# Kernel tuning notes

Hardware: AMD Instinct MI355X
Metric: run time of the kernel (lower is better)

The kernel has to match this reference:

```python
import jax, jax.numpy as jnp
import numpy as np

H = 128          # hidden_dim
NC = 100000      # num_cst
NV = 100000      # num_val
E = 1600000      # num edges
EPS = 1e-5


def _layernorm(x, g, b):
    mu = x.mean(-1, keepdims=True)
    var = x.var(-1, keepdims=True)
    return (x - mu) / jnp.sqrt(var + EPS) * g + b


def setup_inputs() -> dict:
    key = jax.random.key(0)
    ks = jax.random.split(key, 16)
    s = 0.05
    return {
        "x_val": jax.random.normal(ks[0], (NV, H), jnp.float32),
        "r_cst": jax.random.normal(ks[1], (NC, H), jnp.float32),
        "cst_edges": jax.random.randint(ks[2], (2, E), 0, NC, dtype=jnp.int32),
        "LE": jax.random.randint(ks[3], (E,), 0, 2, dtype=jnp.int32),
        "PE": jax.random.randint(ks[4], (E,), 0, 2, dtype=jnp.int32),
        "num_cst": NC,
        "num_val": NV,
        # cst_send: Linear(H,H,bias) -> ReLU -> Linear(H,4H,no bias) -> LayerNorm(4H)
        "W1": jax.random.normal(ks[5], (H, H), jnp.float32) * s,
        "b1": jax.random.normal(ks[6], (H,), jnp.float32) * s,
        "W2": jax.random.normal(ks[7], (H, 4 * H), jnp.float32) * s,
        "g1": jnp.ones((4 * H,), jnp.float32),
        "bt1": jnp.zeros((4 * H,), jnp.float32),
        # val_rec: Linear(H,H,bias) -> ReLU -> Linear(H,H,no bias) -> LayerNorm(H)
        "W3": jax.random.normal(ks[8], (H, H), jnp.float32) * s,
        "b3": jax.random.normal(ks[9], (H,), jnp.float32) * s,
        "W4": jax.random.normal(ks[10], (H, H), jnp.float32) * s,
        "g2": jnp.ones((H,), jnp.float32),
        "bt2": jnp.zeros((H,), jnp.float32),
    }


def reference(x_val, r_cst, cst_edges, LE, PE, num_cst, num_val,
              W1, b1, W2, g1, bt1, W3, b3, W4, g2, bt2):
    # cst_send MLP: [NC, H] -> [NC, 4H], LayerNorm over 4H, then view as [4*NC, H]
    m = _layernorm(jnp.maximum(r_cst @ W1 + b1, 0.0) @ W2, g1, bt1)
    m = m.reshape(4 * num_cst, H)
    # each edge picks one of the 4 message slots of its constraint
    out_idx = 4 * cst_edges[0] + 2 * LE + PE   # [E]
    in_idx = cst_edges[1]                      # [E]
    msg = m[out_idx]                           # [E, H] gather
    r_val = jax.ops.segment_sum(msg, in_idx, num_segments=num_val)  # [NV, H]
    # val_rec MLP on (x_val + r_val) with residual
    h = x_val + r_val
    return _layernorm(jnp.maximum(h @ W3 + b3, 0.0) @ W4, g2, bt2) + x_val
```

## Files before the change

### kernel.cpp

```cpp
#include <hip/hip_runtime.h>
#include <hip/hip_bf16.h>

#define H 128
#define H4 512
#define BM 16

typedef __bf16 bf16x8 __attribute__((ext_vector_type(8)));
typedef float f32x4 __attribute__((ext_vector_type(4)));

__device__ inline f32x4 mfma16(bf16x8 a, bf16x8 b, f32x4 c) {
  return __builtin_amdgcn_mfma_f32_16x16x32_bf16(a, b, c, 0, 0, 0);
}

__global__ __launch_bounds__(256) void pack_kernel(const float* __restrict__ W, int K, int N,
                                                   __bf16* __restrict__ hi,
                                                   __bf16* __restrict__ lo) {
  int idx = blockIdx.x * 256 + threadIdx.x;
  int total = (N >> 4) * (K >> 5) * 64;
  if (idx >= total) return;
  int lane = idx & 63;
  int tile = idx >> 6;
  int KT = K >> 5;
  int nt = tile / KT, kt = tile - nt * KT;
  int col = nt * 16 + (lane & 15);
  int k0 = kt * 32 + (lane >> 4) * 8;
#pragma unroll
  for (int i = 0; i < 8; ++i) {
    float x = W[(long)(k0 + i) * N + col];
    __bf16 h = (__bf16)x;
    hi[(long)idx * 8 + i] = h;
    lo[(long)idx * 8 + i] = (__bf16)(x - (float)h);
  }
}

__global__ __launch_bounds__(256) void copy_kernel(const float4* __restrict__ src,
                                                   float4* __restrict__ dst, int n4) {
  int i = blockIdx.x * 256 + threadIdx.x;
  int stride = gridDim.x * 256;
  for (; i < n4; i += stride) dst[i] = src[i];
}

__global__ __launch_bounds__(256) void cst_mlp_mfma(
    const float* __restrict__ r_cst,
    const __bf16* __restrict__ W1h, const __bf16* __restrict__ W1l,
    const float* __restrict__ b1,
    const __bf16* __restrict__ W2h, const __bf16* __restrict__ W2l,
    const float* __restrict__ g1, const float* __restrict__ bt1,
    float* __restrict__ m) {
  __shared__ float As[BM][132];
  __shared__ float Cs[BM][132];
  __shared__ float Ds[BM][H4];
  __shared__ float mu_s[BM], rs_s[BM];

  const int tid = threadIdx.x;
  const int wave = tid >> 6, lane = tid & 63;
  const long row0 = (long)blockIdx.x * BM;

  {
    const float4* src = (const float4*)(r_cst + row0 * H);
#pragma unroll
    for (int i = 0; i < 2; ++i) {
      int idx = tid + i * 256;
      int r = idx >> 5, c4 = idx & 31;
      *(float4*)&As[r][c4 * 4] = src[idx];
    }
  }
  __syncthreads();

  const int fr = lane & 15;
  const int fk = (lane >> 4) * 8;
  const int rowb = (lane >> 4) * 4;

  bf16x8 a_hi[4], a_lo[4];
#pragma unroll
  for (int kt = 0; kt < 4; ++kt) {
    const float* p = &As[fr][kt * 32 + fk];
    float4 u = *(const float4*)p, v = *(const float4*)(p + 4);
    float vals[8] = {u.x, u.y, u.z, u.w, v.x, v.y, v.z, v.w};
#pragma unroll
    for (int i = 0; i < 8; ++i) {
      __bf16 hh = (__bf16)vals[i];
      a_hi[kt][i] = hh;
      a_lo[kt][i] = (__bf16)(vals[i] - (float)hh);
    }
  }

#pragma unroll
  for (int t = 0; t < 2; ++t) {
    const int nt = wave * 2 + t;
    f32x4 acc = {0.f, 0.f, 0.f, 0.f};
#pragma unroll
    for (int kt = 0; kt < 4; ++kt) {
      const long fi = (long)((nt * 4 + kt) * 64 + lane) * 8;
      bf16x8 bh = *(const bf16x8*)(W1h + fi);
      bf16x8 bl = *(const bf16x8*)(W1l + fi);
      acc = mfma16(a_hi[kt], bh, acc);
      acc = mfma16(a_lo[kt], bh, acc);
      acc = mfma16(a_hi[kt], bl, acc);
    }
    const int col = nt * 16 + fr;
    const float bb = b1[col];
#pragma unroll
    for (int r = 0; r < 4; ++r) Cs[rowb + r][col] = fmaxf(acc[r] + bb, 0.f);
  }
  __syncthreads();

  bf16x8 c_hi[4], c_lo[4];
#pragma unroll
  for (int kt = 0; kt < 4; ++kt) {
    const float* p = &Cs[fr][kt * 32 + fk];
    float4 u = *(const float4*)p, v = *(const float4*)(p + 4);
    float vals[8] = {u.x, u.y, u.z, u.w, v.x, v.y, v.z, v.w};
#pragma unroll
    for (int i = 0; i < 8; ++i) {
      __bf16 hh = (__bf16)vals[i];
      c_hi[kt][i] = hh;
      c_lo[kt][i] = (__bf16)(vals[i] - (float)hh);
    }
  }

#pragma unroll
  for (int t = 0; t < 8; ++t) {
    const int nt = wave * 8 + t;
    f32x4 acc = {0.f, 0.f, 0.f, 0.f};
#pragma unroll
    for (int kt = 0; kt < 4; ++kt) {
      const long fi = (long)((nt * 4 + kt) * 64 + lane) * 8;
      bf16x8 bh = *(const bf16x8*)(W2h + fi);
      bf16x8 bl = *(const bf16x8*)(W2l + fi);
      acc = mfma16(c_hi[kt], bh, acc);
      acc = mfma16(c_lo[kt], bh, acc);
      acc = mfma16(c_hi[kt], bl, acc);
    }
    const int col = nt * 16 + fr;
#pragma unroll
    for (int r = 0; r < 4; ++r) Ds[rowb + r][col] = acc[r];
  }
  __syncthreads();

  {
    for (int r = wave * 4; r < wave * 4 + 4; ++r) {
      float s = 0.f, q = 0.f;
      const float4* rowp = (const float4*)&Ds[r][0];
#pragma unroll
      for (int i = 0; i < 2; ++i) {
        float4 v = rowp[lane * 2 + i];
        s += v.x + v.y + v.z + v.w;
        q += v.x * v.x + v.y * v.y + v.z * v.z + v.w * v.w;
      }
#pragma unroll
      for (int off = 32; off; off >>= 1) {
        s += __shfl_xor(s, off);
        q += __shfl_xor(q, off);
      }
      if (lane == 0) {
        float mu = s * (1.f / H4);
        mu_s[r] = mu;
        rs_s[r] = rsqrtf(q * (1.f / H4) - mu * mu + 1e-5f);
      }
    }
  }
  __syncthreads();

  {
    float4* out4 = (float4*)(m + row0 * H4);
    const float4* D4 = (const float4*)&Ds[0][0];
    const float4* g4 = (const float4*)g1;
    const float4* b4 = (const float4*)bt1;
#pragma unroll
    for (int it = 0; it < 8; ++it) {
      int e4 = tid + it * 256;
      int r = e4 >> 7;
      int c4 = e4 & 127;
      float4 v = D4[e4];
      float4 g = g4[c4], b = b4[c4];
      float mu = mu_s[r], rs = rs_s[r];
      float4 o;
      o.x = (v.x - mu) * rs * g.x + b.x;
      o.y = (v.y - mu) * rs * g.y + b.y;
      o.z = (v.z - mu) * rs * g.z + b.z;
      o.w = (v.w - mu) * rs * g.w + b.w;
      out4[e4] = o;
    }
  }
}

__global__ __launch_bounds__(256) void val_mlp_mfma(
    const float* h, const float* __restrict__ x_val,
    const __bf16* __restrict__ W3h, const __bf16* __restrict__ W3l,
    const float* __restrict__ b3,
    const __bf16* __restrict__ W4h, const __bf16* __restrict__ W4l,
    const float* __restrict__ g2, const float* __restrict__ bt2,
    float* out) {
  __shared__ float As[BM][132];
  __shared__ float Cs[BM][132];
  __shared__ float Ds[BM][H];
  __shared__ float mu_s[BM], rs_s[BM];

  const int tid = threadIdx.x;
  const int wave = tid >> 6, lane = tid & 63;
  const long row0 = (long)blockIdx.x * BM;

  {
    const float4* src = (const float4*)(h + row0 * H);
#pragma unroll
    for (int i = 0; i < 2; ++i) {
      int idx = tid + i * 256;
      int r = idx >> 5, c4 = idx & 31;
      *(float4*)&As[r][c4 * 4] = src[idx];
    }
  }
  __syncthreads();

  const int fr = lane & 15;
  const int fk = (lane >> 4) * 8;
  const int rowb = (lane >> 4) * 4;

  bf16x8 a_hi[4], a_lo[4];
#pragma unroll
  for (int kt = 0; kt < 4; ++kt) {
    const float* p = &As[fr][kt * 32 + fk];
    float4 u = *(const float4*)p, v = *(const float4*)(p + 4);
    float vals[8] = {u.x, u.y, u.z, u.w, v.x, v.y, v.z, v.w};
#pragma unroll
    for (int i = 0; i < 8; ++i) {
      __bf16 hh = (__bf16)vals[i];
      a_hi[kt][i] = hh;
      a_lo[kt][i] = (__bf16)(vals[i] - (float)hh);
    }
  }

#pragma unroll
  for (int t = 0; t < 2; ++t) {
    const int nt = wave * 2 + t;
    f32x4 acc = {0.f, 0.f, 0.f, 0.f};
#pragma unroll
    for (int kt = 0; kt < 4; ++kt) {
      const long fi = (long)((nt * 4 + kt) * 64 + lane) * 8;
      bf16x8 bh = *(const bf16x8*)(W3h + fi);
      bf16x8 bl = *(const bf16x8*)(W3l + fi);
      acc = mfma16(a_hi[kt], bh, acc);
      acc = mfma16(a_lo[kt], bh, acc);
      acc = mfma16(a_hi[kt], bl, acc);
    }
    const int col = nt * 16 + fr;
    const float bb = b3[col];
#pragma unroll
    for (int r = 0; r < 4; ++r) Cs[rowb + r][col] = fmaxf(acc[r] + bb, 0.f);
  }
  __syncthreads();

  bf16x8 c_hi[4], c_lo[4];
#pragma unroll
  for (int kt = 0; kt < 4; ++kt) {
    const float* p = &Cs[fr][kt * 32 + fk];
    float4 u = *(const float4*)p, v = *(const float4*)(p + 4);
    float vals[8] = {u.x, u.y, u.z, u.w, v.x, v.y, v.z, v.w};
#pragma unroll
    for (int i = 0; i < 8; ++i) {
      __bf16 hh = (__bf16)vals[i];
      c_hi[kt][i] = hh;
      c_lo[kt][i] = (__bf16)(vals[i] - (float)hh);
    }
  }

#pragma unroll
  for (int t = 0; t < 2; ++t) {
    const int nt = wave * 2 + t;
    f32x4 acc = {0.f, 0.f, 0.f, 0.f};
#pragma unroll
    for (int kt = 0; kt < 4; ++kt) {
      const long fi = (long)((nt * 4 + kt) * 64 + lane) * 8;
      bf16x8 bh = *(const bf16x8*)(W4h + fi);
      bf16x8 bl = *(const bf16x8*)(W4l + fi);
      acc = mfma16(c_hi[kt], bh, acc);
      acc = mfma16(c_lo[kt], bh, acc);
      acc = mfma16(c_hi[kt], bl, acc);
    }
    const int col = nt * 16 + fr;
#pragma unroll
    for (int r = 0; r < 4; ++r) Ds[rowb + r][col] = acc[r];
  }
  __syncthreads();

  {
    for (int r = wave * 4; r < wave * 4 + 4; ++r) {
      float2 v = *(const float2*)&Ds[r][lane * 2];
      float s = v.x + v.y, q = v.x * v.x + v.y * v.y;
#pragma unroll
      for (int off = 32; off; off >>= 1) {
        s += __shfl_xor(s, off);
        q += __shfl_xor(q, off);
      }
      if (lane == 0) {
        float mu = s * (1.f / H);
        mu_s[r] = mu;
        rs_s[r] = rsqrtf(q * (1.f / H) - mu * mu + 1e-5f);
      }
    }
  }
  __syncthreads();

  {
    float4* out4 = (float4*)(out + row0 * H);
    const float4* x4 = (const float4*)(x_val + row0 * H);
    const float4* D4 = (const float4*)&Ds[0][0];
    const float4* g4 = (const float4*)g2;
    const float4* b4 = (const float4*)bt2;
#pragma unroll
    for (int it = 0; it < 2; ++it) {
      int e4 = tid + it * 256;
      int r = e4 >> 5;
      int c4 = e4 & 31;
      float4 v = D4[e4];
      float4 g = g4[c4], b = b4[c4], xv = x4[e4];
      float mu = mu_s[r], rs = rs_s[r];
      float4 o;
      o.x = (v.x - mu) * rs * g.x + b.x + xv.x;
      o.y = (v.y - mu) * rs * g.y + b.y + xv.y;
      o.z = (v.z - mu) * rs * g.z + b.z + xv.z;
      o.w = (v.w - mu) * rs * g.w + b.w + xv.w;
      out4[e4] = o;
    }
  }
}

__global__ __launch_bounds__(256) void cst_mlp_kernel(
    const float* __restrict__ r_cst,
    const float* __restrict__ W1, const float* __restrict__ b1,
    const float* __restrict__ W2, const float* __restrict__ g1,
    const float* __restrict__ bt1, float* __restrict__ m) {
  __shared__ float As[BM][H];
  __shared__ float Cs[BM][H];
  __shared__ float Ds[BM][H4];
  __shared__ float mu_s[BM], rs_s[BM];
  const int tid = threadIdx.x;
  const long row0 = (long)blockIdx.x * BM;
  {
    const float4* src = (const float4*)(r_cst + row0 * H);
    float4* dst = (float4*)&As[0][0];
#pragma unroll
    for (int i = 0; i < 2; ++i) dst[tid + i * 256] = src[tid + i * 256];
  }
  __syncthreads();
  {
    const int j = tid & (H - 1);
    const int r0 = (tid >> 7) * 8;
    float acc[8] = {0, 0, 0, 0, 0, 0, 0, 0};
#pragma unroll 4
    for (int k = 0; k < H; ++k) {
      float w = W1[k * H + j];
#pragma unroll
      for (int r = 0; r < 8; ++r) acc[r] = fmaf(As[r0 + r][k], w, acc[r]);
    }
    float bb = b1[j];
#pragma unroll
    for (int r = 0; r < 8; ++r) Cs[r0 + r][j] = fmaxf(acc[r] + bb, 0.f);
  }
  __syncthreads();
  {
    const int j = tid * 2;
    float acc[BM][2];
#pragma unroll
    for (int r = 0; r < BM; ++r) acc[r][0] = acc[r][1] = 0.f;
    for (int k = 0; k < H; k += 4) {
      float4 c[BM];
#pragma unroll
      for (int r = 0; r < BM; ++r) c[r] = *(const float4*)&Cs[r][k];
#pragma unroll
      for (int kk = 0; kk < 4; ++kk) {
        const float2 w = *(const float2*)&W2[(k + kk) * H4 + j];
#pragma unroll
        for (int r = 0; r < BM; ++r) {
          float cv = (&c[r].x)[kk];
          acc[r][0] = fmaf(cv, w.x, acc[r][0]);
          acc[r][1] = fmaf(cv, w.y, acc[r][1]);
        }
      }
    }
#pragma unroll
    for (int r = 0; r < BM; ++r) {
      Ds[r][j] = acc[r][0];
      Ds[r][j + 1] = acc[r][1];
    }
  }
  __syncthreads();
  {
    const int wv = tid >> 6, lane = tid & 63;
    for (int r = wv * 4; r < wv * 4 + 4; ++r) {
      float s = 0.f, q = 0.f;
      const float4* rowp = (const float4*)&Ds[r][0];
#pragma unroll
      for (int i = 0; i < 2; ++i) {
        float4 v = rowp[lane * 2 + i];
        s += v.x + v.y + v.z + v.w;
        q += v.x * v.x + v.y * v.y + v.z * v.z + v.w * v.w;
      }
#pragma unroll
      for (int off = 32; off; off >>= 1) {
        s += __shfl_xor(s, off);
        q += __shfl_xor(q, off);
      }
      if (lane == 0) {
        float mu = s * (1.f / H4);
        mu_s[r] = mu;
        rs_s[r] = rsqrtf(q * (1.f / H4) - mu * mu + 1e-5f);
      }
    }
  }
  __syncthreads();
  {
    float4* out4 = (float4*)(m + row0 * H4);
    const float4* D4 = (const float4*)&Ds[0][0];
    const float4* g4 = (const float4*)g1;
    const float4* b4 = (const float4*)bt1;
#pragma unroll
    for (int it = 0; it < 8; ++it) {
      int e4 = tid + it * 256;
      int r = e4 >> 7;
      int c4 = e4 & 127;
      float4 v = D4[e4];
      float4 g = g4[c4], b = b4[c4];
      float mu = mu_s[r], rs = rs_s[r];
      float4 o;
      o.x = (v.x - mu) * rs * g.x + b.x;
      o.y = (v.y - mu) * rs * g.y + b.y;
      o.z = (v.z - mu) * rs * g.z + b.z;
      o.w = (v.w - mu) * rs * g.w + b.w;
      out4[e4] = o;
    }
  }
}

__global__ __launch_bounds__(256) void val_mlp_kernel(
    const float* h, const float* __restrict__ x_val,
    const float* __restrict__ W3, const float* __restrict__ b3,
    const float* __restrict__ W4, const float* __restrict__ g2,
    const float* __restrict__ bt2, float* out) {
  __shared__ float As[BM][H];
  __shared__ float Cs[BM][H];
  __shared__ float Ds[BM][H];
  __shared__ float mu_s[BM], rs_s[BM];
  const int tid = threadIdx.x;
  const long row0 = (long)blockIdx.x * BM;
  {
    const float4* src = (const float4*)(h + row0 * H);
    float4* dst = (float4*)&As[0][0];
#pragma unroll
    for (int i = 0; i < 2; ++i) dst[tid + i * 256] = src[tid + i * 256];
  }
  __syncthreads();
  const int j = tid & (H - 1);
  const int r0 = (tid >> 7) * 8;
  {
    float acc[8] = {0, 0, 0, 0, 0, 0, 0, 0};
#pragma unroll 4
    for (int k = 0; k < H; ++k) {
      float w = W3[k * H + j];
#pragma unroll
      for (int r = 0; r < 8; ++r) acc[r] = fmaf(As[r0 + r][k], w, acc[r]);
    }
    float bb = b3[j];
#pragma unroll
    for (int r = 0; r < 8; ++r) Cs[r0 + r][j] = fmaxf(acc[r] + bb, 0.f);
  }
  __syncthreads();
  {
    float acc[8] = {0, 0, 0, 0, 0, 0, 0, 0};
#pragma unroll 4
    for (int k = 0; k < H; ++k) {
      float w = W4[k * H + j];
#pragma unroll
      for (int r = 0; r < 8; ++r) acc[r] = fmaf(Cs[r0 + r][k], w, acc[r]);
    }
#pragma unroll
    for (int r = 0; r < 8; ++r) Ds[r0 + r][j] = acc[r];
  }
  __syncthreads();
  {
    const int wv = tid >> 6, lane = tid & 63;
    for (int r = wv * 4; r < wv * 4 + 4; ++r) {
      float2 v = *(const float2*)&Ds[r][lane * 2];
      float s = v.x + v.y, q = v.x * v.x + v.y * v.y;
#pragma unroll
      for (int off = 32; off; off >>= 1) {
        s += __shfl_xor(s, off);
        q += __shfl_xor(q, off);
      }
      if (lane == 0) {
        float mu = s * (1.f / H);
        mu_s[r] = mu;
        rs_s[r] = rsqrtf(q * (1.f / H) - mu * mu + 1e-5f);
      }
    }
  }
  __syncthreads();
  {
    float4* out4 = (float4*)(out + row0 * H);
    const float4* x4 = (const float4*)(x_val + row0 * H);
    const float4* D4 = (const float4*)&Ds[0][0];
    const float4* g4 = (const float4*)g2;
    const float4* b4 = (const float4*)bt2;
#pragma unroll
    for (int it = 0; it < 2; ++it) {
      int e4 = tid + it * 256;
      int r = e4 >> 5;
      int c4 = e4 & 31;
      float4 v = D4[e4];
      float4 g = g4[c4], b = b4[c4], xv = x4[e4];
      float mu = mu_s[r], rs = rs_s[r];
      float4 o;
      o.x = (v.x - mu) * rs * g.x + b.x + xv.x;
      o.y = (v.y - mu) * rs * g.y + b.y + xv.y;
      o.z = (v.z - mu) * rs * g.z + b.z + xv.z;
      o.w = (v.w - mu) * rs * g.w + b.w + xv.w;
      out4[e4] = o;
    }
  }
}

__global__ __launch_bounds__(256) void count_kernel(const int* __restrict__ e_in,
                                                    int* __restrict__ cnt, int nE) {
  int i = blockIdx.x * 256 + threadIdx.x;
  if (i < nE) atomicAdd(&cnt[e_in[i]], 1);
}

__device__ inline int wave_incl_scan(int x) {
#pragma unroll
  for (int off = 1; off < 64; off <<= 1) {
    int y = __shfl_up(x, off);
    if ((threadIdx.x & 63) >= off) x += y;
  }
  return x;
}

__global__ __launch_bounds__(256) void scan1_kernel(const int* __restrict__ cnt,
                                                    int* __restrict__ offs,
                                                    int* __restrict__ bsums, int n) {
  int i = blockIdx.x * 256 + threadIdx.x;
  int v = (i < n) ? cnt[i] : 0;
  int incl = wave_incl_scan(v);
  __shared__ int wsum[4];
  int wv = threadIdx.x >> 6, lane = threadIdx.x & 63;
  if (lane == 63) wsum[wv] = incl;
  __syncthreads();
  int add = 0;
  for (int w = 0; w < wv; ++w) add += wsum[w];
  if (i < n) offs[i] = incl - v + add;
  if (threadIdx.x == 255) bsums[blockIdx.x] = incl + add;
}

__global__ __launch_bounds__(1024) void scan2_kernel(int* __restrict__ bsums, int nb,
                                                     int* __restrict__ offs, int n, int total) {
  __shared__ int s[1024];
  int t = threadIdx.x;
  int orig = (t < nb) ? bsums[t] : 0;
  s[t] = orig;
  __syncthreads();
  for (int off = 1; off < 1024; off <<= 1) {
    int v = (t >= off) ? s[t - off] : 0;
    __syncthreads();
    s[t] += v;
    __syncthreads();
  }
  if (t < nb) bsums[t] = s[t] - orig;
  if (t == 0) offs[n] = total;
}

__global__ __launch_bounds__(256) void scan3_kernel(int* __restrict__ offs,
                                                    const int* __restrict__ bsums, int n) {
  int i = blockIdx.x * 256 + threadIdx.x;
  if (i < n) offs[i] += bsums[blockIdx.x];
}

__global__ __launch_bounds__(256) void fill_kernel(
    const int* __restrict__ e_out, const int* __restrict__ e_in,
    const int* __restrict__ LE, const int* __restrict__ PE,
    const int* __restrict__ offs, int* __restrict__ cnt2,
    int* __restrict__ msg_row, int nE) {
  int e = blockIdx.x * 256 + threadIdx.x;
  if (e >= nE) return;
  int v = e_in[e];
  int pos = offs[v] + atomicAdd(&cnt2[v], 1);
  msg_row[pos] = 4 * e_out[e] + 2 * LE[e] + PE[e];
}

__global__ __launch_bounds__(256) void gather_kernel(
    const float* __restrict__ m, const float* __restrict__ x_val,
    const int* __restrict__ offs, const int* __restrict__ msg_row,
    float* __restrict__ h, int nv) {
  int v = blockIdx.x * 4 + (threadIdx.x >> 6);
  if (v >= nv) return;
  int lane = threadIdx.x & 63;
  int beg = offs[v], end = offs[v + 1];
  float2 acc = *(const float2*)(x_val + (long)v * H + lane * 2);
  int p = beg;
  for (; p + 3 < end; p += 4) {
    int r0 = msg_row[p];
    int r1 = msg_row[p + 1];
    int r2 = msg_row[p + 2];
    int r3 = msg_row[p + 3];
    float2 a = *(const float2*)(m + (long)r0 * H + lane * 2);
    float2 b = *(const float2*)(m + (long)r1 * H + lane * 2);
    float2 c = *(const float2*)(m + (long)r2 * H + lane * 2);
    float2 d = *(const float2*)(m + (long)r3 * H + lane * 2);
    acc.x += (a.x + b.x) + (c.x + d.x);
    acc.y += (a.y + b.y) + (c.y + d.y);
  }
  for (; p < end; ++p) {
    int r0 = msg_row[p];
    float2 a = *(const float2*)(m + (long)r0 * H + lane * 2);
    acc.x += a.x;
    acc.y += a.y;
  }
  *(float2*)(h + (long)v * H + lane * 2) = acc;
}

__global__ __launch_bounds__(256) void scatter_kernel(
    const float* __restrict__ m, const int* __restrict__ e_out,
    const int* __restrict__ e_in, const int* __restrict__ LE,
    const int* __restrict__ PE, float* h, int nE) {
  int t = blockIdx.x * 256 + threadIdx.x;
  int edge = t >> 5;
  if (edge >= nE) return;
  int lane = t & 31;
  int c0 = e_out[edge];
  int c1 = e_in[edge];
  int oi = 4 * c0 + 2 * LE[edge] + PE[edge];
  float4 v = *(const float4*)(m + (long)oi * H + lane * 4);
  float* dst = h + (long)c1 * H + lane * 4;
  unsafeAtomicAdd(dst + 0, v.x);
  unsafeAtomicAdd(dst + 1, v.y);
  unsafeAtomicAdd(dst + 2, v.z);
  unsafeAtomicAdd(dst + 3, v.w);
}

extern "C" void kernel_launch(void* const* d_in, const int* in_sizes, int n_in,
                              void* d_out, int out_size, void* d_ws, size_t ws_size,
                              hipStream_t stream) {
  const float* x_val = (const float*)d_in[0];
  const float* r_cst = (const float*)d_in[1];
  const int* edges  = (const int*)d_in[2];
  const int* LE     = (const int*)d_in[3];
  const int* PE     = (const int*)d_in[4];
  const float* W1  = (const float*)d_in[7];
  const float* b1  = (const float*)d_in[8];
  const float* W2  = (const float*)d_in[9];
  const float* g1  = (const float*)d_in[10];
  const float* bt1 = (const float*)d_in[11];
  const float* W3  = (const float*)d_in[12];
  const float* b3  = (const float*)d_in[13];
  const float* W4  = (const float*)d_in[14];
  const float* g2  = (const float*)d_in[15];
  const float* bt2 = (const float*)d_in[16];

  const int NV = in_sizes[0] / H;
  const int NC = in_sizes[1] / H;
  const int nE = in_sizes[3];

  float* out  = (float*)d_out;
  float* mbuf = (float*)d_ws;

  const size_t mbytes = (size_t)4 * NC * H * sizeof(float);
  int* offs  = (int*)((char*)d_ws + mbytes);
  int* cnt   = offs + (NV + 1);
  int* cnt2  = cnt + NV;
  int* bsums = cnt2 + NV;
  int* msg_row = bsums + 1024;
  const size_t csr_bytes = ((size_t)(NV + 1) + NV + NV + 1024 + nE) * sizeof(int);
  const size_t need_csr = mbytes + csr_bytes;

  const size_t pack_off = (need_csr + 63) & ~(size_t)63;
  __bf16* W1h = (__bf16*)((char*)d_ws + pack_off);
  __bf16* W1l = W1h + 16384;
  __bf16* W2h = W1l + 16384;
  __bf16* W2l = W2h + 65536;
  __bf16* W3h = W2l + 65536;
  __bf16* W3l = W3h + 16384;
  __bf16* W4h = W3l + 16384;
  __bf16* W4l = W4h + 16384;
  const size_t need_mfma = pack_off + (size_t)(2 * (16384 * 3 + 65536)) * sizeof(__bf16);

  const int nb = (NV + 255) / 256;
  const bool csr_ok = (ws_size >= need_csr) && (nb <= 1024);
  const bool mfma_ok = csr_ok && (ws_size >= need_mfma);

  if (mfma_ok) {
    pack_kernel<<<8, 256, 0, stream>>>(W1, H, H, W1h, W1l);
    pack_kernel<<<32, 256, 0, stream>>>(W2, H, H4, W2h, W2l);
    pack_kernel<<<8, 256, 0, stream>>>(W3, H, H, W3h, W3l);
    pack_kernel<<<8, 256, 0, stream>>>(W4, H, H, W4h, W4l);
    cst_mlp_mfma<<<NC / BM, 256, 0, stream>>>(r_cst, W1h, W1l, b1, W2h, W2l, g1, bt1, mbuf);
  } else {
    cst_mlp_kernel<<<NC / BM, 256, 0, stream>>>(r_cst, W1, b1, W2, g1, bt1, mbuf);
  }

  if (csr_ok) {
    hipMemsetAsync(cnt, 0, (size_t)NV * sizeof(int), stream);
    hipMemsetAsync(cnt2, 0, (size_t)NV * sizeof(int), stream);
    count_kernel<<<(nE + 255) / 256, 256, 0, stream>>>(edges + nE, cnt, nE);
    scan1_kernel<<<nb, 256, 0, stream>>>(cnt, offs, bsums, NV);
    scan2_kernel<<<1, 1024, 0, stream>>>(bsums, nb, offs, NV, nE);
    scan3_kernel<<<nb, 256, 0, stream>>>(offs, bsums, NV);
    fill_kernel<<<(nE + 255) / 256, 256, 0, stream>>>(edges, edges + nE, LE, PE, offs, cnt2,
                                                      msg_row, nE);
    gather_kernel<<<(NV + 3) / 4, 256, 0, stream>>>(mbuf, x_val, offs, msg_row, out, NV);
  } else {
    copy_kernel<<<2048, 256, 0, stream>>>((const float4*)x_val, (float4*)out, NV * H / 4);
    scatter_kernel<<<(nE * 32 + 255) / 256, 256, 0, stream>>>(mbuf, edges, edges + nE, LE, PE,
                                                              out, nE);
  }

  if (mfma_ok) {
    val_mlp_mfma<<<NV / BM, 256, 0, stream>>>(out, x_val, W3h, W3l, b3, W4h, W4l, g2, bt2, out);
  } else {
    val_mlp_kernel<<<NV / BM, 256, 0, stream>>>(out, x_val, W3, b3, W4, g2, bt2, out);
  }
}
```

Baseline: 658.3 us.

## Process 32 rows per block and compute LayerNorm from MFMA registers

Both MFMA MLP kernels now handle two 16-row M tiles per block. Each loaded bf16 weight fragment feeds twice as many MFMAs, which halves weight traffic per row and the number of blocks. The shared-memory Ds staging buffer is removed: LayerNorm sums are reduced from accumulator registers with lane shuffles plus a small per-wave partial table, and outputs are written straight from registers. The trade-off is higher register pressure and global stores in 64-byte column strips instead of fully vectorized float4 rows.

New measurement: 653.7 us. About the same (-0.7%).

```diff
diff --git a/kernel.cpp b/kernel.cpp
--- a/kernel.cpp
+++ b/kernel.cpp
@@ -4,6 +4,7 @@
 #define H 128
 #define H4 512
 #define BM 16
+#define BM2 32
 
 typedef __bf16 bf16x8 __attribute__((ext_vector_type(8)));
 typedef float f32x4 __attribute__((ext_vector_type(4)));
@@ -40,6 +41,17 @@
   for (; i < n4; i += stride) dst[i] = src[i];
 }
 
+__device__ inline void split8(const float* p, bf16x8& hi, bf16x8& lo) {
+  float4 u = *(const float4*)p, v = *(const float4*)(p + 4);
+  float vals[8] = {u.x, u.y, u.z, u.w, v.x, v.y, v.z, v.w};
+#pragma unroll
+  for (int i = 0; i < 8; ++i) {
+    __bf16 hh = (__bf16)vals[i];
+    hi[i] = hh;
+    lo[i] = (__bf16)(vals[i] - (float)hh);
+  }
+}
+
 __global__ __launch_bounds__(256) void cst_mlp_mfma(
     const float* __restrict__ r_cst,
     const __bf16* __restrict__ W1h, const __bf16* __restrict__ W1l,
@@ -47,19 +59,20 @@
     const __bf16* __restrict__ W2h, const __bf16* __restrict__ W2l,
     const float* __restrict__ g1, const float* __restrict__ bt1,
     float* __restrict__ m) {
-  __shared__ float As[BM][132];
-  __shared__ float Cs[BM][132];
-  __shared__ float Ds[BM][H4];
-  __shared__ float mu_s[BM], rs_s[BM];
+  __shared__ float As[BM2][132];
+  __shared__ float Cs[BM2][132];
+  __shared__ float part_s[BM2][4];
+  __shared__ float part_q[BM2][4];
+  __shared__ float mu_s[BM2], rs_s[BM2];
 
   const int tid = threadIdx.x;
   const int wave = tid >> 6, lane = tid & 63;
-  const long row0 = (long)blockIdx.x * BM;
+  const long row0 = (long)blockIdx.x * BM2;
 
   {
     const float4* src = (const float4*)(r_cst + row0 * H);
 #pragma unroll
-    for (int i = 0; i < 2; ++i) {
+    for (int i = 0; i < 4; ++i) {
       int idx = tid + i * 256;
       int r = idx >> 5, c4 = idx & 31;
       *(float4*)&As[r][c4 * 4] = src[idx];
@@ -71,116 +84,115 @@
   const int fk = (lane >> 4) * 8;
   const int rowb = (lane >> 4) * 4;
 
-  bf16x8 a_hi[4], a_lo[4];
-#pragma unroll
-  for (int kt = 0; kt < 4; ++kt) {
-    const float* p = &As[fr][kt * 32 + fk];
-    float4 u = *(const float4*)p, v = *(const float4*)(p + 4);
-    float vals[8] = {u.x, u.y, u.z, u.w, v.x, v.y, v.z, v.w};
-#pragma unroll
-    for (int i = 0; i < 8; ++i) {
-      __bf16 hh = (__bf16)vals[i];
-      a_hi[kt][i] = hh;
-      a_lo[kt][i] = (__bf16)(vals[i] - (float)hh);
-    }
-  }
+  bf16x8 a_hi[2][4], a_lo[2][4];
+#pragma unroll
+  for (int mt = 0; mt < 2; ++mt)
+#pragma unroll
+    for (int kt = 0; kt < 4; ++kt) split8(&As[mt * 16 + fr][kt * 32 + fk], a_hi[mt][kt], a_lo[mt][kt]);
 
 #pragma unroll
   for (int t = 0; t < 2; ++t) {
     const int nt = wave * 2 + t;
-    f32x4 acc = {0.f, 0.f, 0.f, 0.f};
+    f32x4 acc0 = {0.f, 0.f, 0.f, 0.f}, acc1 = {0.f, 0.f, 0.f, 0.f};
 #pragma unroll
     for (int kt = 0; kt < 4; ++kt) {
       const long fi = (long)((nt * 4 + kt) * 64 + lane) * 8;
       bf16x8 bh = *(const bf16x8*)(W1h + fi);
       bf16x8 bl = *(const bf16x8*)(W1l + fi);
-      acc = mfma16(a_hi[kt], bh, acc);
-      acc = mfma16(a_lo[kt], bh, acc);
-      acc = mfma16(a_hi[kt], bl, acc);
+      acc0 = mfma16(a_hi[0][kt], bh, acc0);
+      acc0 = mfma16(a_lo[0][kt], bh, acc0);
+      acc0 = mfma16(a_hi[0][kt], bl, acc0);
+      acc1 = mfma16(a_hi[1][kt], bh, acc1);
+      acc1 = mfma16(a_lo[1][kt], bh, acc1);
+      acc1 = mfma16(a_hi[1][kt], bl, acc1);
     }
     const int col = nt * 16 + fr;
     const float bb = b1[col];
 #pragma unroll
-    for (int r = 0; r < 4; ++r) Cs[rowb + r][col] = fmaxf(acc[r] + bb, 0.f);
-  }
-  __syncthreads();
-
-  bf16x8 c_hi[4], c_lo[4];
-#pragma unroll
-  for (int kt = 0; kt < 4; ++kt) {
-    const float* p = &Cs[fr][kt * 32 + fk];
-    float4 u = *(const float4*)p, v = *(const float4*)(p + 4);
-    float vals[8] = {u.x, u.y, u.z, u.w, v.x, v.y, v.z, v.w};
-#pragma unroll
-    for (int i = 0; i < 8; ++i) {
-      __bf16 hh = (__bf16)vals[i];
-      c_hi[kt][i] = hh;
-      c_lo[kt][i] = (__bf16)(vals[i] - (float)hh);
-    }
-  }
+    for (int r = 0; r < 4; ++r) {
+      Cs[rowb + r][col] = fmaxf(acc0[r] + bb, 0.f);
+      Cs[16 + rowb + r][col] = fmaxf(acc1[r] + bb, 0.f);
+    }
+  }
+  __syncthreads();
+
+  bf16x8 c_hi[2][4], c_lo[2][4];
+#pragma unroll
+  for (int mt = 0; mt < 2; ++mt)
+#pragma unroll
+    for (int kt = 0; kt < 4; ++kt) split8(&Cs[mt * 16 + fr][kt * 32 + fk], c_hi[mt][kt], c_lo[mt][kt]);
+
+  f32x4 d[2][8];
+  float ss[2][4], qq[2][4];
+#pragma unroll
+  for (int mt = 0; mt < 2; ++mt)
+#pragma unroll
+    for (int r = 0; r < 4; ++r) ss[mt][r] = qq[mt][r] = 0.f;
 
 #pragma unroll
   for (int t = 0; t < 8; ++t) {
     const int nt = wave * 8 + t;
-    f32x4 acc = {0.f, 0.f, 0.f, 0.f};
+    f32x4 acc0 = {0.f, 0.f, 0.f, 0.f}, acc1 = {0.f, 0.f, 0.f, 0.f};
 #pragma unroll
     for (int kt = 0; kt < 4; ++kt) {
       const long fi = (long)((nt * 4 + kt) * 64 + lane) * 8;
       bf16x8 bh = *(const bf16x8*)(W2h + fi);
       bf16x8 bl = *(const bf16x8*)(W2l + fi);
-      acc = mfma16(c_hi[kt], bh, acc);
-      acc = mfma16(c_lo[kt], bh, acc);
-      acc = mfma16(c_hi[kt], bl, acc);
-    }
-    const int col = nt * 16 + fr;
-#pragma unroll
-    for (int r = 0; r < 4; ++r) Ds[rowb + r][col] = acc[r];
-  }
-  __syncthreads();
-
-  {
-    for (int r = wave * 4; r < wave * 4 + 4; ++r) {
-      float s = 0.f, q = 0.f;
-      const float4* rowp = (const float4*)&Ds[r][0];
-#pragma unroll
-      for (int i = 0; i < 2; ++i) {
-        float4 v = rowp[lane * 2 + i];
-        s += v.x + v.y + v.z + v.w;
-        q += v.x * v.x + v.y * v.y + v.z * v.z + v.w * v.w;
-      }
-#pragma unroll
-      for (int off = 32; off; off >>= 1) {
+      acc0 = mfma16(c_hi[0][kt], bh, acc0);
+      acc0 = mfma16(c_lo[0][kt], bh, acc0);
+      acc0 = mfma16(c_hi[0][kt], bl, acc0);
+      acc1 = mfma16(c_hi[1][kt], bh, acc1);
+      acc1 = mfma16(c_lo[1][kt], bh, acc1);
+      acc1 = mfma16(c_hi[1][kt], bl, acc1);
+    }
+    d[0][t] = acc0;
+    d[1][t] = acc1;
+#pragma unroll
+    for (int r = 0; r < 4; ++r) {
+      ss[0][r] += acc0[r];
+      qq[0][r] += acc0[r] * acc0[r];
+      ss[1][r] += acc1[r];
+      qq[1][r] += acc1[r] * acc1[r];
+    }
+  }
+
+#pragma unroll
+  for (int mt = 0; mt < 2; ++mt)
+#pragma unroll
+    for (int r = 0; r < 4; ++r) {
+      float s = ss[mt][r], q = qq[mt][r];
+#pragma unroll
+      for (int off = 1; off < 16; off <<= 1) {
         s += __shfl_xor(s, off);
         q += __shfl_xor(q, off);
       }
-      if (lane == 0) {
-        float mu = s * (1.f / H4);
-        mu_s[r] = mu;
-        rs_s[r] = rsqrtf(q * (1.f / H4) - mu * mu + 1e-5f);
-      }
-    }
-  }
-  __syncthreads();
-
-  {
-    float4* out4 = (float4*)(m + row0 * H4);
-    const float4* D4 = (const float4*)&Ds[0][0];
-    const float4* g4 = (const float4*)g1;
-    const float4* b4 = (const float4*)bt1;
-#pragma unroll
-    for (int it = 0; it < 8; ++it) {
-      int e4 = tid + it * 256;
-      int r = e4 >> 7;
-      int c4 = e4 & 127;
-      float4 v = D4[e4];
-      float4 g = g4[c4], b = b4[c4];
-      float mu = mu_s[r], rs = rs_s[r];
-      float4 o;
-      o.x = (v.x - mu) * rs * g.x + b.x;
-      o.y = (v.y - mu) * rs * g.y + b.y;
-      o.z = (v.z - mu) * rs * g.z + b.z;
-      o.w = (v.w - mu) * rs * g.w + b.w;
-      out4[e4] = o;
+      if (fr == 0) {
+        part_s[mt * 16 + rowb + r][wave] = s;
+        part_q[mt * 16 + rowb + r][wave] = q;
+      }
+    }
+  __syncthreads();
+
+  if (tid < BM2) {
+    float s = part_s[tid][0] + part_s[tid][1] + part_s[tid][2] + part_s[tid][3];
+    float q = part_q[tid][0] + part_q[tid][1] + part_q[tid][2] + part_q[tid][3];
+    float mu = s * (1.f / H4);
+    mu_s[tid] = mu;
+    rs_s[tid] = rsqrtf(q * (1.f / H4) - mu * mu + 1e-5f);
+  }
+  __syncthreads();
+
+#pragma unroll
+  for (int t = 0; t < 8; ++t) {
+    const int col = (wave * 8 + t) * 16 + fr;
+    const float g = g1[col], b = bt1[col];
+#pragma unroll
+    for (int mt = 0; mt < 2; ++mt) {
+#pragma unroll
+      for (int r = 0; r < 4; ++r) {
+        const int row = mt * 16 + rowb + r;
+        m[(row0 + row) * H4 + col] = (d[mt][t][r] - mu_s[row]) * rs_s[row] * g + b;
+      }
     }
   }
 }
@@ -192,19 +204,20 @@
     const __bf16* __restrict__ W4h, const __bf16* __restrict__ W4l,
     const float* __restrict__ g2, const float* __restrict__ bt2,
     float* out) {
-  __shared__ float As[BM][132];
-  __shared__ float Cs[BM][132];
-  __shared__ float Ds[BM][H];
-  __shared__ float mu_s[BM], rs_s[BM];
+  __shared__ float As[BM2][132];
+  __shared__ float Cs[BM2][132];
+  __shared__ float part_s[BM2][4];
+  __shared__ float part_q[BM2][4];
+  __shared__ float mu_s[BM2], rs_s[BM2];
 
   const int tid = threadIdx.x;
   const int wave = tid >> 6, lane = tid & 63;
-  const long row0 = (long)blockIdx.x * BM;
+  const long row0 = (long)blockIdx.x * BM2;
 
   {
     const float4* src = (const float4*)(h + row0 * H);
 #pragma unroll
-    for (int i = 0; i < 2; ++i) {
+    for (int i = 0; i < 4; ++i) {
       int idx = tid + i * 256;
       int r = idx >> 5, c4 = idx & 31;
       *(float4*)&As[r][c4 * 4] = src[idx];
@@ -216,111 +229,116 @@
   const int fk = (lane >> 4) * 8;
   const int rowb = (lane >> 4) * 4;
 
-  bf16x8 a_hi[4], a_lo[4];
-#pragma unroll
-  for (int kt = 0; kt < 4; ++kt) {
-    const float* p = &As[fr][kt * 32 + fk];
-    float4 u = *(const float4*)p, v = *(const float4*)(p + 4);
-    float vals[8] = {u.x, u.y, u.z, u.w, v.x, v.y, v.z, v.w};
-#pragma unroll
-    for (int i = 0; i < 8; ++i) {
-      __bf16 hh = (__bf16)vals[i];
-      a_hi[kt][i] = hh;
-      a_lo[kt][i] = (__bf16)(vals[i] - (float)hh);
-    }
-  }
+  bf16x8 a_hi[2][4], a_lo[2][4];
+#pragma unroll
+  for (int mt = 0; mt < 2; ++mt)
+#pragma unroll
+    for (int kt = 0; kt < 4; ++kt) split8(&As[mt * 16 + fr][kt * 32 + fk], a_hi[mt][kt], a_lo[mt][kt]);
 
 #pragma unroll
   for (int t = 0; t < 2; ++t) {
     const int nt = wave * 2 + t;
-    f32x4 acc = {0.f, 0.f, 0.f, 0.f};
+    f32x4 acc0 = {0.f, 0.f, 0.f, 0.f}, acc1 = {0.f, 0.f, 0.f, 0.f};
 #pragma unroll
     for (int kt = 0; kt < 4; ++kt) {
       const long fi = (long)((nt * 4 + kt) * 64 + lane) * 8;
       bf16x8 bh = *(const bf16x8*)(W3h + fi);
       bf16x8 bl = *(const bf16x8*)(W3l + fi);
-      acc = mfma16(a_hi[kt], bh, acc);
-      acc = mfma16(a_lo[kt], bh, acc);
-      acc = mfma16(a_hi[kt], bl, acc);
+      acc0 = mfma16(a_hi[0][kt], bh, acc0);
+      acc0 = mfma16(a_lo[0][kt], bh, acc0);
+      acc0 = mfma16(a_hi[0][kt], bl, acc0);
+      acc1 = mfma16(a_hi[1][kt], bh, acc1);
+      acc1 = mfma16(a_lo[1][kt], bh, acc1);
+      acc1 = mfma16(a_hi[1][kt], bl, acc1);
     }
     const int col = nt * 16 + fr;
     const float bb = b3[col];
 #pragma unroll
-    for (int r = 0; r < 4; ++r) Cs[rowb + r][col] = fmaxf(acc[r] + bb, 0.f);
-  }
-  __syncthreads();
-
-  bf16x8 c_hi[4], c_lo[4];
-#pragma unroll
-  for (int kt = 0; kt < 4; ++kt) {
-    const float* p = &Cs[fr][kt * 32 + fk];
-    float4 u = *(const float4*)p, v = *(const float4*)(p + 4);
-    float vals[8] = {u.x, u.y, u.z, u.w, v.x, v.y, v.z, v.w};
-#pragma unroll
-    for (int i = 0; i < 8; ++i) {
-      __bf16 hh = (__bf16)vals[i];
-      c_hi[kt][i] = hh;
-      c_lo[kt][i] = (__bf16)(vals[i] - (float)hh);
-    }
-  }
+    for (int r = 0; r < 4; ++r) {
+      Cs[rowb + r][col] = fmaxf(acc0[r] + bb, 0.f);
+      Cs[16 + rowb + r][col] = fmaxf(acc1[r] + bb, 0.f);
+    }
+  }
+  __syncthreads();
+
+  bf16x8 c_hi[2][4], c_lo[2][4];
+#pragma unroll
+  for (int mt = 0; mt < 2; ++mt)
+#pragma unroll
+    for (int kt = 0; kt < 4; ++kt) split8(&Cs[mt * 16 + fr][kt * 32 + fk], c_hi[mt][kt], c_lo[mt][kt]);
+
+  f32x4 d[2][2];
+  float ss[2][4], qq[2][4];
+#pragma unroll
+  for (int mt = 0; mt < 2; ++mt)
+#pragma unroll
+    for (int r = 0; r < 4; ++r) ss[mt][r] = qq[mt][r] = 0.f;
 
 #pragma unroll
   for (int t = 0; t < 2; ++t) {
     const int nt = wave * 2 + t;
-    f32x4 acc = {0.f, 0.f, 0.f, 0.f};
+    f32x4 acc0 = {0.f, 0.f, 0.f, 0.f}, acc1 = {0.f, 0.f, 0.f, 0.f};
 #pragma unroll
     for (int kt = 0; kt < 4; ++kt) {
       const long fi = (long)((nt * 4 + kt) * 64 + lane) * 8;
       bf16x8 bh = *(const bf16x8*)(W4h + fi);
       bf16x8 bl = *(const bf16x8*)(W4l + fi);
-      acc = mfma16(c_hi[kt], bh, acc);
-      acc = mfma16(c_lo[kt], bh, acc);
-      acc = mfma16(c_hi[kt], bl, acc);
-    }
-    const int col = nt * 16 + fr;
-#pragma unroll
-    for (int r = 0; r < 4; ++r) Ds[rowb + r][col] = acc[r];
-  }
-  __syncthreads();
-
-  {
-    for (int r = wave * 4; r < wave * 4 + 4; ++r) {
-      float2 v = *(const float2*)&Ds[r][lane * 2];
-      float s = v.x + v.y, q = v.x * v.x + v.y * v.y;
-#pragma unroll
-      for (int off = 32; off; off >>= 1) {
+      acc0 = mfma16(c_hi[0][kt], bh, acc0);
+      acc0 = mfma16(c_lo[0][kt], bh, acc0);
+      acc0 = mfma16(c_hi[0][kt], bl, acc0);
+      acc1 = mfma16(c_hi[1][kt], bh, acc1);
+      acc1 = mfma16(c_lo[1][kt], bh, acc1);
+      acc1 = mfma16(c_hi[1][kt], bl, acc1);
+    }
+    d[0][t] = acc0;
+    d[1][t] = acc1;
+#pragma unroll
+    for (int r = 0; r < 4; ++r) {
+      ss[0][r] += acc0[r];
+      qq[0][r] += acc0[r] * acc0[r];
+      ss[1][r] += acc1[r];
+      qq[1][r] += acc1[r] * acc1[r];
+    }
+  }
+
+#pragma unroll
+  for (int mt = 0; mt < 2; ++mt)
+#pragma unroll
+    for (int r = 0; r < 4; ++r) {
+      float s = ss[mt][r], q = qq[mt][r];
+#pragma unroll
+      for (int off = 1; off < 16; off <<= 1) {
         s += __shfl_xor(s, off);
         q += __shfl_xor(q, off);
       }
-      if (lane == 0) {
-        float mu = s * (1.f / H);
-        mu_s[r] = mu;
-        rs_s[r] = rsqrtf(q * (1.f / H) - mu * mu + 1e-5f);
-      }
-    }
-  }
-  __syncthreads();
-
-  {
-    float4* out4 = (float4*)(out + row0 * H);
-    const float4* x4 = (const float4*)(x_val + row0 * H);
-    const float4* D4 = (const float4*)&Ds[0][0];
-    const float4* g4 = (const float4*)g2;
-    const float4* b4 = (const float4*)bt2;
-#pragma unroll
-    for (int it = 0; it < 2; ++it) {
-      int e4 = tid + it * 256;
-      int r = e4 >> 5;
-      int c4 = e4 & 31;
-      float4 v = D4[e4];
-      float4 g = g4[c4], b = b4[c4], xv = x4[e4];
-      float mu = mu_s[r], rs = rs_s[r];
-      float4 o;
-      o.x = (v.x - mu) * rs * g.x + b.x + xv.x;
-      o.y = (v.y - mu) * rs * g.y + b.y + xv.y;
-      o.z = (v.z - mu) * rs * g.z + b.z + xv.z;
-      o.w = (v.w - mu) * rs * g.w + b.w + xv.w;
-      out4[e4] = o;
+      if (fr == 0) {
+        part_s[mt * 16 + rowb + r][wave] = s;
+        part_q[mt * 16 + rowb + r][wave] = q;
+      }
+    }
+  __syncthreads();
+
+  if (tid < BM2) {
+    float s = part_s[tid][0] + part_s[tid][1] + part_s[tid][2] + part_s[tid][3];
+    float q = part_q[tid][0] + part_q[tid][1] + part_q[tid][2] + part_q[tid][3];
+    float mu = s * (1.f / H);
+    mu_s[tid] = mu;
+    rs_s[tid] = rsqrtf(q * (1.f / H) - mu * mu + 1e-5f);
+  }
+  __syncthreads();
+
+#pragma unroll
+  for (int t = 0; t < 2; ++t) {
+    const int col = (wave * 2 + t) * 16 + fr;
+    const float g = g2[col], b = bt2[col];
+#pragma unroll
+    for (int mt = 0; mt < 2; ++mt) {
+#pragma unroll
+      for (int r = 0; r < 4; ++r) {
+        const int row = mt * 16 + rowb + r;
+        const float xv = x_val[(row0 + row) * H + col];
+        out[(row0 + row) * H + col] = (d[mt][t][r] - mu_s[row]) * rs_s[row] * g + b + xv;
+      }
     }
   }
 }
@@ -683,14 +701,14 @@
 
   const int nb = (NV + 255) / 256;
   const bool csr_ok = (ws_size >= need_csr) && (nb <= 1024);
-  const bool mfma_ok = csr_ok && (ws_size >= need_mfma);
+  const bool mfma_ok = csr_ok && (ws_size >= need_mfma) && (NC % BM2 == 0) && (NV % BM2 == 0);
 
   if (mfma_ok) {
     pack_kernel<<<8, 256, 0, stream>>>(W1, H, H, W1h, W1l);
     pack_kernel<<<32, 256, 0, stream>>>(W2, H, H4, W2h, W2l);
     pack_kernel<<<8, 256, 0, stream>>>(W3, H, H, W3h, W3l);
     pack_kernel<<<8, 256, 0, stream>>>(W4, H, H, W4h, W4l);
-    cst_mlp_mfma<<<NC / BM, 256, 0, stream>>>(r_cst, W1h, W1l, b1, W2h, W2l, g1, bt1, mbuf);
+    cst_mlp_mfma<<<NC / BM2, 256, 0, stream>>>(r_cst, W1h, W1l, b1, W2h, W2l, g1, bt1, mbuf);
   } else {
     cst_mlp_kernel<<<NC / BM, 256, 0, stream>>>(r_cst, W1, b1, W2, g1, bt1, mbuf);
   }
@@ -712,7 +730,7 @@
   }
 
   if (mfma_ok) {
-    val_mlp_mfma<<<NV / BM, 256, 0, stream>>>(out, x_val, W3h, W3l, b3, W4h, W4l, g2, bt2, out);
+    val_mlp_mfma<<<NV / BM2, 256, 0, stream>>>(out, x_val, W3h, W3l, b3, W4h, W4l, g2, bt2, out);
   } else {
     val_mlp_kernel<<<NV / BM, 256, 0, stream>>>(out, x_val, W3, b3, W4, g2, bt2, out);
   }
```
